# Optimization experiments

Hardware: AMD Instinct MI355X
Metric: run time of the kernel (lower is better)

Reference implementation:

```python
import jax, jax.numpy as jnp
import numpy as np

N_NODE = 100000
DEG = 16
N_EDGE = N_NODE * DEG
IN_C = 64
HID_C = 64
N_REL = 8


def setup_inputs() -> dict:
    key = jax.random.key(0)
    ks = jax.random.split(key, 6)
    x = jax.random.normal(ks[0], (N_NODE, IN_C), dtype=jnp.float32)
    # glorot-scale relation weights [num_rel, in_channels, hidden_channels]
    scale = np.sqrt(6.0 / (IN_C + HID_C)).astype(np.float32)
    W = jax.random.uniform(ks[1], (N_REL, IN_C, HID_C), dtype=jnp.float32,
                           minval=-scale, maxval=scale)
    # CSR row pointer: fixed degree DEG per destination node
    ptr = (jnp.arange(N_NODE + 1, dtype=jnp.int32) * DEG)
    idx = jax.random.randint(ks[2], (N_EDGE,), 0, N_NODE, dtype=jnp.int32)
    edge_types = jax.random.randint(ks[3], (N_EDGE,), 0, N_REL, dtype=jnp.int32)
    count = jnp.ones((N_REL,), dtype=jnp.int32)  # unused by forward
    history_map = jnp.where(jax.random.uniform(ks[4], (N_NODE,)) < 0.1,
                            jnp.int32(0), jnp.int32(-1))
    history_buffer = jax.random.normal(ks[5], (N_NODE, HID_C), dtype=jnp.float32)
    used_mask = jnp.ones((N_NODE,), dtype=bool)  # unused by forward
    return {
        "x": x, "W": W, "ptr": ptr, "idx": idx, "edge_types": edge_types,
        "count": count, "history_map": history_map,
        "history_buffer": history_buffer, "used_mask": used_mask,
        "history_size": 64, "num_node": N_NODE,
    }


def reference(x, W, ptr, idx, edge_types, count, history_map,
              history_buffer, used_mask, history_size, num_node):
    # RGCNOP: out[i] = sum_{e in [ptr[i],ptr[i+1])} x[idx[e]] @ W[edge_types[e]]
    # Pre-transform per relation (same math, fewer FLOPs): x_r = x @ W[r]
    xr = jnp.einsum('ni,rio->rno', x, W)          # [R, N, hid]
    msg = xr[edge_types, idx]                     # per-edge gather [E, hid]
    E = idx.shape[0]
    # destination node of each edge from CSR ptr
    dst = jnp.searchsorted(ptr, jnp.arange(E, dtype=ptr.dtype), side='right') - 1
    out = jax.ops.segment_sum(msg, dst, num_segments=num_node)  # [N, hid]
    # degree normalization
    deg = (ptr[1:] - ptr[:-1]).astype(out.dtype)
    out = out / deg[:, None]
    # conditional history-buffer overwrite
    if history_size > 0:
        out = jnp.where((history_map != -1)[:, None], history_buffer, out)
    his = out
    return (out, his)
```

## Files before the change

### kernel.cpp

```cpp
#include <hip/hip_runtime.h>
#include <hip/hip_bf16.h>

#define NNODE 100000
#define CIN   64
#define CHID  64
#define NREL  8
#define NGRP  6250

typedef __attribute__((ext_vector_type(8))) short bf16x8;
typedef __attribute__((ext_vector_type(4))) float f32x4;
typedef unsigned long long u64;

__device__ __forceinline__ unsigned short f2bf(float f) {
    __hip_bfloat16 h = __float2bfloat16(f);
    return __builtin_bit_cast(unsigned short, h);
}
__device__ __forceinline__ float bf2f(unsigned short u) {
    unsigned int v = ((unsigned int)u) << 16;
    return __builtin_bit_cast(float, v);
}
__device__ __forceinline__ float f8tof(unsigned char b) {
    return __builtin_amdgcn_cvt_f32_fp8((unsigned int)b, 0);
}

__global__ void k_prep_x(const float* __restrict__ x, unsigned int* __restrict__ xb) {
    int i = blockIdx.x * 256 + threadIdx.x;
    if (i >= NNODE * CIN / 4) return;
    float4 v = *reinterpret_cast<const float4*>(x + (size_t)i * 4);
    int p = __builtin_amdgcn_cvt_pk_fp8_f32(v.x, v.y, 0, false);
    p = __builtin_amdgcn_cvt_pk_fp8_f32(v.z, v.w, p, true);
    xb[i] = (unsigned int)p;
}

__global__ void k_sort(const int* __restrict__ ptr, const int* __restrict__ idx,
                       const int* __restrict__ et, int* __restrict__ sidx,
                       u64* __restrict__ typ4) {
    int node = blockIdx.x * 256 + threadIdx.x;
    if (node >= NNODE) return;
    int eb = ptr[node], en = ptr[node + 1];
    if (en - eb != 16) { typ4[node] = 0; return; }
    u64 cnt = 0;
#pragma unroll
    for (int ee = 0; ee < 16; ++ee)
        cnt += 1ull << (8 * et[eb + ee]);
    u64 pre = cnt * 0x0101010101010100ull;
    u64 occ = 0, tp = 0;
#pragma unroll
    for (int ee = 0; ee < 16; ++ee) {
        int te = et[eb + ee];
        int sh = te * 8;
        int pos = (int)((pre >> sh) & 0xFF) + (int)((occ >> sh) & 0xFF);
        occ += 1ull << sh;
        sidx[eb + pos] = idx[eb + ee];
        tp |= (u64)te << (4 * pos);
    }
    typ4[node] = tp;
}

__global__ void k_prep_w(const float* __restrict__ W, unsigned short* __restrict__ wf) {
    int tid = blockIdx.x * 256 + threadIdx.x;
    if (tid >= 64 * 64) return;
    int tile = tid >> 6, lane = tid & 63;
    int kt = tile >> 2, nt = tile & 3;
    int kbase = kt * 32 + (lane >> 4) * 8;
    int col = nt * 16 + (lane & 15);
    unsigned short v[8];
#pragma unroll
    for (int j = 0; j < 8; ++j)
        v[j] = f2bf(W[(kbase + j) * 64 + col]);
    ushort4* dst = reinterpret_cast<ushort4*>(wf + (size_t)tid * 8);
    ushort4 lo, hi;
    lo.x = v[0]; lo.y = v[1]; lo.z = v[2]; lo.w = v[3];
    hi.x = v[4]; hi.y = v[5]; hi.z = v[6]; hi.w = v[7];
    dst[0] = lo; dst[1] = hi;
}

__launch_bounds__(256, 8)
__global__ void k_main(const unsigned char* __restrict__ xb,
                       const bf16x8* __restrict__ wf,
                       const int* __restrict__ ptr,
                       const int* __restrict__ sidx,
                       const u64* __restrict__ typ4,
                       const int* __restrict__ idx,
                       const int* __restrict__ et,
                       const int* __restrict__ hmap,
                       const float* __restrict__ hbuf,
                       float* __restrict__ out) {
    __shared__ __align__(16) unsigned short S[8192];

    int wave = __builtin_amdgcn_readfirstlane((int)(threadIdx.x >> 6));
    int lane = threadIdx.x & 63;
    int n0 = blockIdx.x * 16;
    int nbase = n0 + wave * 4;
    char* sb = reinterpret_cast<char*>(&S[0]);

    {
        f32x4 z = {0.f, 0.f, 0.f, 0.f};
        f32x4* sz = reinterpret_cast<f32x4*>(sb);
        sz[threadIdx.x]       = z;
        sz[threadIdx.x + 256] = z;
        sz[threadIdx.x + 512] = z;
        sz[threadIdx.x + 768] = z;
    }
    __syncthreads();

    int ebX = nbase * 16;
    int eb0 = ptr[nbase + 0], eb1 = ptr[nbase + 1], eb2 = ptr[nbase + 2],
        eb3 = ptr[nbase + 3], eb4 = ptr[nbase + 4];
    bool fixed16 = (eb0 == ebX) && (eb1 == ebX + 16) && (eb2 == ebX + 32) &&
                   (eb3 == ebX + 48) && (eb4 == ebX + 64);

    if (fixed16) {
        const int* sp = sidx + ebX;
        u64 tp0 = typ4[nbase + 0], tp1 = typ4[nbase + 1],
            tp2 = typ4[nbase + 2], tp3 = typ4[nbase + 3];

        unsigned char xvA[16], xvB[16];
        int sA[16], sB[16];

#define SLOAD(sarr, nn)                                                       \
        _Pragma("unroll")                                                     \
        for (int ee = 0; ee < 16; ++ee) sarr[ee] = sp[(nn) * 16 + ee];
#define LOADN(buf, sarr)                                                      \
        _Pragma("unroll")                                                     \
        for (int ee = 0; ee < 16; ++ee)                                       \
            buf[ee] = xb[(size_t)(unsigned)sarr[ee] * 64 + lane];
#define FLUSHACC(buf, nn, tp)                                                 \
        {                                                                     \
            int row_ = wave * 4 + (nn);                                       \
            unsigned int vlx_ = ((unsigned int)lane * 2u)                     \
                                ^ (((unsigned int)(row_ & 7)) << 4);          \
            unsigned int rb_ = (unsigned int)row_ * 1024u;                    \
            float s_ = 0.f;                                                   \
            _Pragma("unroll")                                                 \
            for (int ee = 0; ee < 16; ++ee) {                                 \
                s_ += f8tof(buf[ee]);                                         \
                int tcur_ = (int)((tp >> (4 * ee)) & 0xF);                    \
                int tnxt_ = (ee == 15) ? 16 : (int)((tp >> (4 * ee + 4)) & 0xF); \
                if (tcur_ != tnxt_) {                                         \
                    unsigned int byte_ = rb_ + (unsigned int)tcur_ * 128u + vlx_; \
                    *reinterpret_cast<unsigned short*>(sb + byte_) = f2bf(s_); \
                    s_ = 0.f;                                                 \
                }                                                             \
            }                                                                 \
        }

        SLOAD(sA, 0); LOADN(xvA, sA);
        SLOAD(sB, 1); LOADN(xvB, sB);
        SLOAD(sA, 2); FLUSHACC(xvA, 0, tp0); LOADN(xvA, sA);
        SLOAD(sB, 3); FLUSHACC(xvB, 1, tp1); LOADN(xvB, sB);
        FLUSHACC(xvA, 2, tp2);
        FLUSHACC(xvB, 3, tp3);
#undef SLOAD
#undef LOADN
#undef FLUSHACC
    } else {
        int l16 = lane & 15;
        int ebs[5] = {eb0, eb1, eb2, eb3, eb4};
        for (int nn = 0; nn < 4; ++nn) {
            int eb = ebs[nn], en = ebs[nn + 1];
            float s0=0.f,s1=0.f,s2=0.f,s3=0.f,s4=0.f,s5=0.f,s6=0.f,s7=0.f;
            for (int e = eb; e < en; e += 16) {
                int m = en - e; if (m > 16) m = 16;
                int vi = 0, vt = 0;
                if (l16 < m) { vi = idx[e + l16]; vt = et[e + l16]; }
                for (int ee = 0; ee < m; ++ee) {
                    int src = __builtin_amdgcn_readlane(vi, ee);
                    int t   = __builtin_amdgcn_readlane(vt, ee);
                    float v = f8tof(xb[(size_t)(unsigned)src * 64 + lane]);
                    if      (t == 0) s0 += v;
                    else if (t == 1) s1 += v;
                    else if (t == 2) s2 += v;
                    else if (t == 3) s3 += v;
                    else if (t == 4) s4 += v;
                    else if (t == 5) s5 += v;
                    else if (t == 6) s6 += v;
                    else             s7 += v;
                }
            }
            int row = wave * 4 + nn;
            unsigned int vlx = ((unsigned int)lane * 2u)
                               ^ (((unsigned int)(row & 7)) << 4);
            unsigned int rb = (unsigned int)row * 1024u;
            float sv[8] = {s0,s1,s2,s3,s4,s5,s6,s7};
#pragma unroll
            for (int r = 0; r < 8; ++r) {
                unsigned int byte = rb + (unsigned int)r * 128u + vlx;
                *reinterpret_cast<unsigned short*>(sb + byte) = f2bf(sv[r]);
            }
        }
    }
    __syncthreads();

    int nt = wave;
    f32x4 acc = {0.f,0.f,0.f,0.f};
    unsigned int arow  = (unsigned int)(lane & 15);
    unsigned int abase = arow * 1024u + (unsigned int)((lane >> 4) * 16);
    unsigned int axor  = (arow & 7u) << 4;
#pragma unroll 4
    for (int kt = 0; kt < 16; ++kt) {
        unsigned int abyte = (abase + (unsigned int)kt * 64u) ^ axor;
        bf16x8 a = *reinterpret_cast<const bf16x8*>(sb + abyte);
        bf16x8 b = wf[(kt * 4 + nt) * 64 + lane];
        acc = __builtin_amdgcn_mfma_f32_16x16x32_bf16(a, b, acc, 0, 0, 0);
    }

    int col   = nt * 16 + (lane & 15);
    int rquad = (lane >> 4) * 4;
#pragma unroll
    for (int j = 0; j < 4; ++j) {
        int node = n0 + rquad + j;
        float invd = 1.0f / (float)(ptr[node + 1] - ptr[node]);
        float v = acc[j] * invd;
        if (hmap[node] != -1) v = hbuf[node * 64 + col];
        out[node * 64 + col] = v;
        out[NNODE * 64 + node * 64 + col] = v;
    }
}

extern "C" void kernel_launch(void* const* d_in, const int* in_sizes, int n_in,
                              void* d_out, int out_size, void* d_ws, size_t ws_size,
                              hipStream_t stream) {
    (void)in_sizes; (void)n_in; (void)out_size; (void)ws_size;
    const float* x    = (const float*)d_in[0];
    const float* W    = (const float*)d_in[1];
    const int*   ptr  = (const int*)d_in[2];
    const int*   idx  = (const int*)d_in[3];
    const int*   et   = (const int*)d_in[4];
    const int*   hmap = (const int*)d_in[6];
    const float* hbuf = (const float*)d_in[7];
    float* out = (float*)d_out;

    char* w = (char*)d_ws;
    unsigned char*  xb  = (unsigned char*)w;
    unsigned short* wfu = (unsigned short*)(w + 6400000);
    int*            sidx= (int*)(w + 6465536);
    u64*            tp4 = (u64*)(w + 12865536);

    k_prep_x<<<dim3(6250), dim3(256), 0, stream>>>(x, (unsigned int*)xb);
    k_sort<<<dim3((NNODE + 255) / 256), dim3(256), 0, stream>>>(ptr, idx, et, sidx, tp4);
    k_prep_w<<<dim3(16), dim3(256), 0, stream>>>(W, wfu);
    k_main<<<dim3(NGRP), dim3(256), 0, stream>>>(
        xb, (const bf16x8*)wfu, ptr, sidx, tp4, idx, et, hmap, hbuf, out);
}
```

Measured before the change: 68.04 us.

## Gather 4 fp8 channels per lane with dword loads across 4 nodes per wave

The fixed-degree path is restructured so each wave processes its four nodes in parallel, 16 lanes per node. Each lane loads a 32-bit word holding four fp8 channels and converts them with packed conversions. The sorted source indices are staged through LDS and read back as int4 vectors. Per-relation partial sums are written as packed 8-byte LDS stores. This cuts the number of gather instructions per lane and the byte-granular memory traffic, at the cost of more registers and an extra LDS round-trip for the indices.

```diff
diff --git a/kernel.cpp b/kernel.cpp
--- a/kernel.cpp
+++ b/kernel.cpp
@@ -9,6 +9,7 @@
 
 typedef __attribute__((ext_vector_type(8))) short bf16x8;
 typedef __attribute__((ext_vector_type(4))) float f32x4;
+typedef __attribute__((ext_vector_type(2))) float f32x2;
 typedef unsigned long long u64;
 
 __device__ __forceinline__ unsigned short f2bf(float f) {
@@ -19,8 +20,9 @@
     unsigned int v = ((unsigned int)u) << 16;
     return __builtin_bit_cast(float, v);
 }
-__device__ __forceinline__ float f8tof(unsigned char b) {
-    return __builtin_amdgcn_cvt_f32_fp8((unsigned int)b, 0);
+template <int SEL>
+__device__ __forceinline__ float f8tof(unsigned int w) {
+    return __builtin_amdgcn_cvt_f32_fp8(w, SEL);
 }
 
 __global__ void k_prep_x(const float* __restrict__ x, unsigned int* __restrict__ xb) {
@@ -87,6 +89,7 @@
                        const float* __restrict__ hbuf,
                        float* __restrict__ out) {
     __shared__ __align__(16) unsigned short S[8192];
+    __shared__ __align__(16) int VS[4][64];
 
     int wave = __builtin_amdgcn_readfirstlane((int)(threadIdx.x >> 6));
     int lane = threadIdx.x & 63;
@@ -111,49 +114,61 @@
                    (eb3 == ebX + 48) && (eb4 == ebX + 64);
 
     if (fixed16) {
-        const int* sp = sidx + ebX;
+        VS[wave][lane] = sidx[ebX + lane];
+
         u64 tp0 = typ4[nbase + 0], tp1 = typ4[nbase + 1],
             tp2 = typ4[nbase + 2], tp3 = typ4[nbase + 3];
 
-        unsigned char xvA[16], xvB[16];
-        int sA[16], sB[16];
-
-#define SLOAD(sarr, nn)                                                       \
-        _Pragma("unroll")                                                     \
-        for (int ee = 0; ee < 16; ++ee) sarr[ee] = sp[(nn) * 16 + ee];
-#define LOADN(buf, sarr)                                                      \
-        _Pragma("unroll")                                                     \
-        for (int ee = 0; ee < 16; ++ee)                                       \
-            buf[ee] = xb[(size_t)(unsigned)sarr[ee] * 64 + lane];
-#define FLUSHACC(buf, nn, tp)                                                 \
+        int g = lane >> 4;
+        u64 tpg = (g == 0) ? tp0 : ((g == 1) ? tp1 : ((g == 2) ? tp2 : tp3));
+        int row = wave * 4 + g;
+        unsigned int rowxor  = ((unsigned int)(row & 7)) << 4;
+        unsigned int rowbase = (unsigned int)row * 1024u;
+        unsigned int chb     = (unsigned int)(lane & 15) * 8u;
+        unsigned int choff   = (unsigned int)(lane & 15) * 4u;
+
+        const int* vsp = &VS[wave][g * 16];
+        int4 q0 = *reinterpret_cast<const int4*>(vsp);
+        int4 q1 = *reinterpret_cast<const int4*>(vsp + 4);
+        int4 q2 = *reinterpret_cast<const int4*>(vsp + 8);
+        int4 q3 = *reinterpret_cast<const int4*>(vsp + 12);
+
+#define LD(s) (*reinterpret_cast<const unsigned int*>( \
+                   xb + (size_t)(((unsigned int)(s)) * 64u + choff)))
+        unsigned int d0  = LD(q0.x), d1  = LD(q0.y), d2  = LD(q0.z), d3  = LD(q0.w);
+        unsigned int d4  = LD(q1.x), d5  = LD(q1.y), d6  = LD(q1.z), d7  = LD(q1.w);
+        unsigned int d8  = LD(q2.x), d9  = LD(q2.y), d10 = LD(q2.z), d11 = LD(q2.w);
+        unsigned int d12 = LD(q3.x), d13 = LD(q3.y), d14 = LD(q3.z), d15 = LD(q3.w);
+#undef LD
+
+        float s0 = 0.f, s1 = 0.f, s2 = 0.f, s3 = 0.f;
+
+#define STEP(ee, dd)                                                          \
         {                                                                     \
-            int row_ = wave * 4 + (nn);                                       \
-            unsigned int vlx_ = ((unsigned int)lane * 2u)                     \
-                                ^ (((unsigned int)(row_ & 7)) << 4);          \
-            unsigned int rb_ = (unsigned int)row_ * 1024u;                    \
-            float s_ = 0.f;                                                   \
-            _Pragma("unroll")                                                 \
-            for (int ee = 0; ee < 16; ++ee) {                                 \
-                s_ += f8tof(buf[ee]);                                         \
-                int tcur_ = (int)((tp >> (4 * ee)) & 0xF);                    \
-                int tnxt_ = (ee == 15) ? 16 : (int)((tp >> (4 * ee + 4)) & 0xF); \
-                if (tcur_ != tnxt_) {                                         \
-                    unsigned int byte_ = rb_ + (unsigned int)tcur_ * 128u + vlx_; \
-                    *reinterpret_cast<unsigned short*>(sb + byte_) = f2bf(s_); \
-                    s_ = 0.f;                                                 \
-                }                                                             \
+            f32x2 plo = __builtin_amdgcn_cvt_pk_f32_fp8((int)(dd), false);    \
+            f32x2 phi = __builtin_amdgcn_cvt_pk_f32_fp8((int)(dd), true);     \
+            s0 += plo[0]; s1 += plo[1]; s2 += phi[0]; s3 += phi[1];           \
+            int tcur = (int)((tpg >> ((4 * (ee)) & 63)) & 0xF);               \
+            int tnxt = ((ee) == 15) ? 16                                      \
+                                    : (int)((tpg >> ((4 * (ee) + 4) & 63)) & 0xF); \
+            if (tcur != tnxt) {                                               \
+                unsigned int lo = (unsigned int)f2bf(s0)                      \
+                                | ((unsigned int)f2bf(s1) << 16);             \
+                unsigned int hi = (unsigned int)f2bf(s2)                      \
+                                | ((unsigned int)f2bf(s3) << 16);             \
+                unsigned int byte = (rowbase + (unsigned int)tcur * 128u + chb) \
+                                    ^ rowxor;                                 \
+                uint2 pk; pk.x = lo; pk.y = hi;                               \
+                *reinterpret_cast<uint2*>(sb + byte) = pk;                    \
+                s0 = 0.f; s1 = 0.f; s2 = 0.f; s3 = 0.f;                       \
             }                                                                 \
         }
 
-        SLOAD(sA, 0); LOADN(xvA, sA);
-        SLOAD(sB, 1); LOADN(xvB, sB);
-        SLOAD(sA, 2); FLUSHACC(xvA, 0, tp0); LOADN(xvA, sA);
-        SLOAD(sB, 3); FLUSHACC(xvB, 1, tp1); LOADN(xvB, sB);
-        FLUSHACC(xvA, 2, tp2);
-        FLUSHACC(xvB, 3, tp3);
-#undef SLOAD
-#undef LOADN
-#undef FLUSHACC
+        STEP(0, d0);   STEP(1, d1);   STEP(2, d2);   STEP(3, d3);
+        STEP(4, d4);   STEP(5, d5);   STEP(6, d6);   STEP(7, d7);
+        STEP(8, d8);   STEP(9, d9);   STEP(10, d10); STEP(11, d11);
+        STEP(12, d12); STEP(13, d13); STEP(14, d14); STEP(15, d15);
+#undef STEP
     } else {
         int l16 = lane & 15;
         int ebs[5] = {eb0, eb1, eb2, eb3, eb4};
@@ -167,7 +182,7 @@
                 for (int ee = 0; ee < m; ++ee) {
                     int src = __builtin_amdgcn_readlane(vi, ee);
                     int t   = __builtin_amdgcn_readlane(vt, ee);
-                    float v = f8tof(xb[(size_t)(unsigned)src * 64 + lane]);
+                    float v = f8tof<0>((unsigned int)xb[(size_t)(unsigned)src * 64 + lane]);
                     if      (t == 0) s0 += v;
                     else if (t == 1) s1 += v;
                     else if (t == 2) s2 += v;
```

Result: faster. 64.87 us (-4.7%).
